# Optimization experiments

Measured on AMD Instinct MI355X. Metric: run time of the kernel, lower is better.

## Reference

```python
import jax, jax.numpy as jnp
import numpy as np
from jax import lax

NEG = -1.0e9


def setup_inputs() -> dict:
    key = jax.random.key(0)
    ks = jax.random.split(key, 12)
    B, S, d, H = 4, 1024, 1024, 16
    sc = 1.0 / np.sqrt(d)
    inp = {
        "query": jax.random.normal(ks[0], (B, S, d), jnp.float32),
        "key": jax.random.normal(ks[1], (B, S, d), jnp.float32),
        "value": jax.random.normal(ks[2], (B, S, d), jnp.float32),
        # causal mask: True = masked (future positions)
        "mask": jnp.triu(jnp.ones((S, S), bool), k=1)[None, None],
        "Wq": jax.random.normal(ks[3], (d, d), jnp.float32) * sc,
        "bq": jnp.zeros((d,), jnp.float32),
        "Wk": jax.random.normal(ks[4], (d, d), jnp.float32) * sc,
        "bk": jnp.zeros((d,), jnp.float32),
        "Wv": jax.random.normal(ks[5], (d, d), jnp.float32) * sc,
        "bv": jnp.zeros((d,), jnp.float32),
        "Wo": jax.random.normal(ks[6], (d, d), jnp.float32) * sc,
        "bo": jnp.zeros((d,), jnp.float32),
        "gammas": jax.random.uniform(ks[7], (H, 1, 1), jnp.float32, -0.05, 0.05),
    }
    return inp


def reference(query, key, value, mask, Wq, bq, Wk, bk, Wv, bv, Wo, bo, gammas):
    B, S, d = query.shape
    H = gammas.shape[0]
    dk = d // H

    def proj(x, W, b):
        # [B,S,d] -> [B,H,S,dk]
        return (x @ W.T + b).reshape(B, S, H, dk).transpose(0, 2, 1, 3)

    q = proj(query, Wq, bq)
    k = proj(key, Wk, bk)
    v = proj(value, Wv, bv)

    scores = jnp.einsum("bhqd,bhkd->bhqk", q, k) / np.float32(np.sqrt(dk))

    # --- distance-decay effect (no-grad block in torch) ---
    p = jax.nn.softmax(jnp.where(mask, NEG, scores), axis=-1)
    distcum = jnp.cumsum(p, axis=-1)
    disttot = jnp.sum(p, axis=-1, keepdims=True)
    idx = jnp.arange(S, dtype=scores.dtype)
    pos = jnp.abs(idx[:, None] - idx[None, :])[None, None]  # [1,1,S,S]
    dist = jnp.sqrt(jnp.clip((disttot - distcum) * pos, 0.0))
    dist = lax.stop_gradient(dist)

    gamma = -jnp.abs(gammas)[None]  # [1,H,1,1]
    total_effect = jnp.clip(jnp.exp(dist * gamma), 1e-5, 1e5)

    gated = jnp.where(mask, NEG, scores * total_effect)
    attn = jax.nn.softmax(gated, axis=-1)
    attn = jnp.where(mask, 0.0, attn)

    out = jnp.einsum("bhqk,bhkd->bhqd", attn, v)
    out = out.transpose(0, 2, 1, 3).reshape(B, S, d)
    out = out @ Wo.T + bo
    return out, attn
```

## Files before the change

### kernel.cpp

```cpp
#include <hip/hip_runtime.h>
#include <hip/hip_bf16.h>

typedef __attribute__((ext_vector_type(8))) short short8;
typedef __attribute__((ext_vector_type(4))) float f32x4;
typedef __attribute__((ext_vector_type(4))) unsigned short us4;

#define MFMA(a, b, c) __builtin_amdgcn_mfma_f32_16x16x32_bf16((a), (b), (c), 0, 0, 0)

static __device__ inline unsigned short f2b(float f) {
    __hip_bfloat16 h = __float2bfloat16(f);
    return *reinterpret_cast<unsigned short*>(&h);
}
static __device__ inline float b2f(unsigned short u) {
    unsigned int x = ((unsigned int)u) << 16;
    return __builtin_bit_cast(float, x);
}

static __device__ __forceinline__ void gload_lds16(const unsigned short* g, unsigned short* s) {
    __builtin_amdgcn_global_load_lds(
        (const __attribute__((address_space(1))) unsigned int*)(g),
        (__attribute__((address_space(3))) unsigned int*)(s),
        16, 0, 0);
}
#define WAITV(N) asm volatile("s_waitcnt vmcnt(" #N ")" ::: "memory")
#define WAITL    asm volatile("s_waitcnt lgkmcnt(0)" ::: "memory")
#define SBAR     __builtin_amdgcn_s_barrier()
#define SCHED0   __builtin_amdgcn_sched_barrier(0)

__global__ __launch_bounds__(256) void convk(
    const float* __restrict__ i0, const float* __restrict__ i1,
    const float* __restrict__ i2, const float* __restrict__ i3,
    unsigned short* o0, unsigned short* o1, unsigned short* o2, unsigned short* o3, int n)
{
    const float* in; unsigned short* out;
    switch (blockIdx.y) {
        case 0: in = i0; out = o0; break;
        case 1: in = i1; out = o1; break;
        case 2: in = i2; out = o2; break;
        default: in = i3; out = o3; break;
    }
    int i = (blockIdx.x * 256 + threadIdx.x) * 4;
    if (i >= n) return;
    float4 v = *(const float4*)(in + i);
    us4 o;
    o[0] = f2b(v.x); o[1] = f2b(v.y); o[2] = f2b(v.z); o[3] = f2b(v.w);
    *(us4*)(out + i) = o;
}

__global__ __launch_bounds__(256) void gemm_qkv(
    const float* __restrict__ Aq, const float* __restrict__ Ak, const float* __restrict__ Av,
    const unsigned short* __restrict__ wq, const unsigned short* __restrict__ wk,
    const unsigned short* __restrict__ wv,
    const float* __restrict__ bq, const float* __restrict__ bk, const float* __restrict__ bv,
    unsigned short* __restrict__ qh, unsigned short* __restrict__ kh,
    unsigned short* __restrict__ vt,
    int M, int N, int K)
{
    __shared__ unsigned short sA[3][2 * 64 * 32];
    __shared__ unsigned short sB[3][2 * 128 * 32];

    const int d  = blockIdx.x;
    const int c  = d & 7;
    const int t  = d >> 3;
    const int nn = t & 7;
    const int gq = t >> 3;
    const int g  = gq * 8 + c;
    const int z  = g >> 6;
    const int mm = g & 63;

    const float* A           = z == 0 ? Aq : z == 1 ? Ak : Av;
    const unsigned short* Bm = z == 0 ? wq : z == 1 ? wk : wv;
    const float* bias        = z == 0 ? bq : z == 1 ? bk : bv;
    unsigned short* Cb       = z == 0 ? qh : z == 1 ? kh : vt;
    const int emode          = z == 2 ? 2 : 1;

    const int tid = threadIdx.x;
    const int wave = tid >> 6, lane = tid & 63;
    const int wm = (wave >> 1) * 32, wn = (wave & 1) * 64;
    const int bm = mm * 64, bn = nn * 128;
    const int fr = lane & 15, fg = lane >> 4;

    const int ar = tid >> 2, ac = (tid & 3) * 16;
    const float* Ag = A + (size_t)(bm + ar) * K + ac;
    const int aks = ac >> 5, acol = ac & 31;
    const int brow = lane >> 2, bchk = (lane & 3) * 8;
    const unsigned short* Bg = Bm + (size_t)(bn + wave * 32 + brow) * K + bchk;

    f32x4 acc[2][4] = {};
    const int nt = K >> 6;

    float4 rA[4];
    #define LOAD_A(t)  { const float* p = Ag + ((t) << 6); \
        rA[0] = *(const float4*)(p); rA[1] = *(const float4*)(p + 4); \
        rA[2] = *(const float4*)(p + 8); rA[3] = *(const float4*)(p + 12); }
    #define GLOAD_B(buf, t) { const unsigned short* p = Bg + ((t) << 6); \
        gload_lds16(p,               &sB[buf][(0 * 128 + wave * 32 + 0 ) * 32]); \
        gload_lds16(p + 16 * K,      &sB[buf][(0 * 128 + wave * 32 + 16) * 32]); \
        gload_lds16(p + 32,          &sB[buf][(1 * 128 + wave * 32 + 0 ) * 32]); \
        gload_lds16(p + 16 * K + 32, &sB[buf][(1 * 128 + wave * 32 + 16) * 32]); }
    #define WRITE_A(buf) { \
        unsigned short* dsts = &sA[buf][(aks * 64 + ar) * 32 + acol]; \
        us4 w0, w1; \
        w0[0] = f2b(rA[0].x); w0[1] = f2b(rA[0].y); w0[2] = f2b(rA[0].z); w0[3] = f2b(rA[0].w); \
        w1[0] = f2b(rA[1].x); w1[1] = f2b(rA[1].y); w1[2] = f2b(rA[1].z); w1[3] = f2b(rA[1].w); \
        *(us4*)(dsts) = w0; *(us4*)(dsts + 4) = w1; \
        w0[0] = f2b(rA[2].x); w0[1] = f2b(rA[2].y); w0[2] = f2b(rA[2].z); w0[3] = f2b(rA[2].w); \
        w1[0] = f2b(rA[3].x); w1[1] = f2b(rA[3].y); w1[2] = f2b(rA[3].z); w1[3] = f2b(rA[3].w); \
        *(us4*)(dsts + 8) = w0; *(us4*)(dsts + 12) = w1; }

    LOAD_A(0);
    SCHED0;
    GLOAD_B(0, 0);
    WAITV(4);
    WRITE_A(0);
    LOAD_A(1);
    SCHED0;
    GLOAD_B(1, 1);

    for (int t = 0; t < nt; ++t) {
        const int cur = t % 3;
        if (t + 1 < nt) { WAITV(4); } else { WAITV(0); }
        if (t + 1 < nt) { WRITE_A((t + 1) % 3); }
        if (t + 2 < nt) {
            LOAD_A(t + 2);
            SCHED0;
            GLOAD_B((t + 2) % 3, t + 2);
        }
        WAITL;
        SBAR; SCHED0;

        short8 af[2][2], bf[4][2];
        #pragma unroll
        for (int ks = 0; ks < 2; ++ks) {
            #pragma unroll
            for (int mr = 0; mr < 2; ++mr)
                af[mr][ks] = *(const short8*)&sA[cur][(ks * 64 + wm + mr * 16 + fr) * 32 + fg * 8];
            #pragma unroll
            for (int nr = 0; nr < 4; ++nr)
                bf[nr][ks] = *(const short8*)&sB[cur][(ks * 128 + wn + nr * 16 + fr) * 32 + fg * 8];
        }
        #pragma unroll
        for (int ks = 0; ks < 2; ++ks)
            #pragma unroll
            for (int mr = 0; mr < 2; ++mr)
                #pragma unroll
                for (int nr = 0; nr < 4; ++nr)
                    acc[mr][nr] = MFMA(af[mr][ks], bf[nr][ks], acc[mr][nr]);

        SCHED0; SBAR;
    }

    #pragma unroll
    for (int mr = 0; mr < 2; ++mr)
        #pragma unroll
        for (int nr = 0; nr < 4; ++nr)
            #pragma unroll
            for (int j = 0; j < 4; ++j) {
                int m = bm + wm + mr * 16 + fg * 4 + j;
                int n = bn + wn + nr * 16 + fr;
                float v = acc[mr][nr][j] + bias[n];
                int b = m >> 10, s = m & 1023, h = n >> 6, dc = n & 63;
                if (emode == 1)
                    Cb[(((size_t)(b * 16 + h)) * 1024 + s) * 64 + dc] = f2b(v);
                else
                    Cb[(((size_t)(b * 16 + h)) * 64 + dc) * 1024 + s] = f2b(v);
            }
    #undef LOAD_A
    #undef GLOAD_B
    #undef WRITE_A
}

__global__ __launch_bounds__(256) void gemm_wo(
    const unsigned short* __restrict__ A, const unsigned short* __restrict__ Bm,
    const float* __restrict__ bias, float* __restrict__ Cf, int M, int N, int K)
{
    __shared__ unsigned short sA[3][2 * 64 * 32];
    __shared__ unsigned short sB[3][2 * 128 * 32];

    const int d  = blockIdx.x;
    const int c  = d & 7;
    const int t0 = d >> 3;
    const int nn = t0 & 7;
    const int gq = t0 >> 3;
    const int mm = gq * 8 + c;

    const int tid = threadIdx.x;
    const int wave = tid >> 6, lane = tid & 63;
    const int wm = (wave >> 1) * 32, wn = (wave & 1) * 64;
    const int bm = mm * 64, bn = nn * 128;
    const int fr = lane & 15, fg = lane >> 4;

    const int srow = lane >> 2, schk = (lane & 3) * 8;
    const unsigned short* Ag = A + (size_t)(bm + wave * 16 + srow) * K + schk;
    const unsigned short* Bg = Bm + (size_t)(bn + wave * 32 + srow) * K + schk;

    #define STAGE(buf, t) { const unsigned short* ap = Ag + ((t) << 6); \
        gload_lds16(ap,      &sA[buf][(0 * 64 + wave * 16) * 32]); \
        gload_lds16(ap + 32, &sA[buf][(1 * 64 + wave * 16) * 32]); \
        const unsigned short* bp = Bg + ((t) << 6); \
        gload_lds16(bp,               &sB[buf][(0 * 128 + wave * 32 + 0 ) * 32]); \
        gload_lds16(bp + 16 * K,      &sB[buf][(0 * 128 + wave * 32 + 16) * 32]); \
        gload_lds16(bp + 32,          &sB[buf][(1 * 128 + wave * 32 + 0 ) * 32]); \
        gload_lds16(bp + 16 * K + 32, &sB[buf][(1 * 128 + wave * 32 + 16) * 32]); }

    f32x4 acc[2][4] = {};
    const int nt = K >> 6;

    STAGE(0, 0); STAGE(1, 1);
    for (int t = 0; t < nt; ++t) {
        const int cur = t % 3;
        if (t + 2 < nt)      { STAGE((t + 2) % 3, t + 2); WAITV(12); }
        else if (t + 1 < nt) { WAITV(6); }
        else                 { WAITV(0); }
        SBAR; SCHED0;

        short8 af[2][2], bf[4][2];
        #pragma unroll
        for (int ks = 0; ks < 2; ++ks) {
            #pragma unroll
            for (int mr = 0; mr < 2; ++mr)
                af[mr][ks] = *(const short8*)&sA[cur][(ks * 64 + wm + mr * 16 + fr) * 32 + fg * 8];
            #pragma unroll
            for (int nr = 0; nr < 4; ++nr)
                bf[nr][ks] = *(const short8*)&sB[cur][(ks * 128 + wn + nr * 16 + fr) * 32 + fg * 8];
        }
        #pragma unroll
        for (int ks = 0; ks < 2; ++ks)
            #pragma unroll
            for (int mr = 0; mr < 2; ++mr)
                #pragma unroll
                for (int nr = 0; nr < 4; ++nr)
                    acc[mr][nr] = MFMA(af[mr][ks], bf[nr][ks], acc[mr][nr]);

        SCHED0; SBAR;
    }
    #undef STAGE

    #pragma unroll
    for (int mr = 0; mr < 2; ++mr)
        #pragma unroll
        for (int nr = 0; nr < 4; ++nr)
            #pragma unroll
            for (int j = 0; j < 4; ++j) {
                int m = bm + wm + mr * 16 + fg * 4 + j;
                int n = bn + wn + nr * 16 + fr;
                Cf[(size_t)m * N + n] = acc[mr][nr][j] + bias[n];
            }
}

__global__ __launch_bounds__(256) void attn_fused(
    const unsigned short* __restrict__ Qh,
    const unsigned short* __restrict__ Kh,
    const unsigned short* __restrict__ Vt,
    const float* __restrict__ gammas,
    float* __restrict__ attn_out,
    unsigned short* __restrict__ ctx)
{
    extern __shared__ char smem[];
    const int RS = 1032;
    unsigned short* s_s = (unsigned short*)smem;
    unsigned short* s_q = (unsigned short*)(smem + 16 * RS * 2);
    float* s_inv = (float*)(smem + 16 * RS * 2 + 16 * 72 * 2);
    const int S = 1024;

    int gid = blockIdx.y * gridDim.x + blockIdx.x;
    int jj = gid >> 3;
    const int bh = (gid & 7) * 8 + (jj >> 6);
    const int qb = jj & 63;
    const int q0 = qb * 16;
    const int tid = threadIdx.x;
    const int wave = tid >> 6, lane = tid & 63, fr = lane & 15, fg = lane >> 4;

    {
        int rr = tid >> 4, c4 = (tid & 15) * 4;
        *(uint2*)&s_q[rr * 72 + c4] = *(const uint2*)&Qh[((size_t)bh * S + q0 + rr) * 64 + c4];
    }
    __syncthreads();
    const int kmax = q0 + 15;

    {
        short8 qf0 = *(const short8*)&s_q[fr * 72 + fg * 8];
        short8 qf1 = *(const short8*)&s_q[fr * 72 + 32 + fg * 8];
        const unsigned short* kbase = &Kh[(size_t)bh * S * 64];
        for (int nf = 0; nf < 16; ++nf) {
            int cb = (nf * 4 + wave) * 16;
            if (cb > kmax) break;
            const unsigned short* kb = kbase + (size_t)cb * 64;
            short8 kf0 = *(const short8*)&kb[fr * 64 + fg * 8];
            short8 kf1 = *(const short8*)&kb[fr * 64 + 32 + fg * 8];
            f32x4 a = {0.f, 0.f, 0.f, 0.f};
            a = MFMA(qf0, kf0, a);
            a = MFMA(qf1, kf1, a);
            #pragma unroll
            for (int j = 0; j < 4; ++j)
                s_s[(size_t)(fg * 4 + j) * RS + cb + fr] = f2b(a[j] * 0.125f);
        }
    }
    __syncthreads();

    {
        const int r = tid >> 4, sub = tid & 15;
        const int qr = q0 + r;
        unsigned short* srow = &s_s[(size_t)r * RS];
        const float ag = fabsf(gammas[bh & 15]);
        const int m = ((qb + 4) >> 2) | 1;
        const int L = 4 * m;
        const int base = sub * L;

        float seg = 0.f;
        for (int c = 0; c < m; ++c) {
            us4 s4 = *(const us4*)&srow[base + c * 4];
            #pragma unroll
            for (int j = 0; j < 4; ++j) {
                int kk = base + c * 4 + j;
                seg += (kk <= qr) ? __expf(b2f(s4[j])) : 0.f;
            }
        }
        float x = seg, t;
        t = __shfl_up(x, 1, 16); if (sub >= 1) x += t;
        t = __shfl_up(x, 2, 16); if (sub >= 2) x += t;
        t = __shfl_up(x, 4, 16); if (sub >= 4) x += t;
        t = __shfl_up(x, 8, 16); if (sub >= 8) x += t;
        const float T = __shfl(x, 15, 16);
        const float invT = 1.f / T;
        float run = x - seg;

        float ls2 = 0.f;
        for (int c = 0; c < m; ++c) {
            us4 s4 = *(const us4*)&srow[base + c * 4];
            us4 o;
            #pragma unroll
            for (int j = 0; j < 4; ++j) {
                int kk = base + c * 4 + j;
                bool act = kk <= qr;
                float s = b2f(s4[j]);
                float e = act ? __expf(s) : 0.f;
                run += e;
                float rem = fmaxf(T - run, 0.f) * invT;
                float dist = sqrtf(rem * (float)(qr - kk));
                float te = __expf(-ag * dist);
                float e2 = act ? __expf(s * te) : 0.f;
                o[j] = f2b(e2);
                ls2 += e2;
            }
            *(us4*)&srow[base + c * 4] = o;
        }
        us4 z = {0, 0, 0, 0};
        for (int c = 4 * L + sub; c < 256; c += 16)
            *(us4*)&srow[c * 4] = z;
        #pragma unroll
        for (int mm = 1; mm < 16; mm <<= 1) ls2 += __shfl_xor(ls2, mm, 16);
        if (sub == 0) s_inv[r] = 1.f / ls2;
    }
    __syncthreads();

    for (int r2 = 0; r2 < 16; ++r2) {
        us4 e4 = *(const us4*)&s_s[(size_t)r2 * RS + tid * 4];
        float iv = s_inv[r2];
        f32x4 w = {b2f(e4[0]) * iv, b2f(e4[1]) * iv, b2f(e4[2]) * iv, b2f(e4[3]) * iv};
        __builtin_nontemporal_store(w,
            (f32x4*)(attn_out + ((size_t)bh * S + q0 + r2) * S + tid * 4));
    }

    {
        const unsigned short* vb = &Vt[(size_t)bh * 64 * S];
        f32x4 acc = {0.f, 0.f, 0.f, 0.f};
        const int ktiles = (kmax + 32) >> 5;
        const unsigned short* prow = &s_s[(size_t)fr * RS];
        for (int kt = 0; kt < ktiles; ++kt) {
            short8 pa = *(const short8*)&prow[kt * 32 + fg * 8];
            short8 vf = *(const short8*)&vb[(size_t)(wave * 16 + fr) * S + kt * 32 + fg * 8];
            acc = MFMA(pa, vf, acc);
        }
        int b = bh >> 4, h = bh & 15;
        #pragma unroll
        for (int j = 0; j < 4; ++j) {
            float iv = s_inv[fg * 4 + j];
            ctx[((size_t)b * S + q0 + fg * 4 + j) * 1024 + h * 64 + wave * 16 + fr] = f2b(acc[j] * iv);
        }
    }
}

extern "C" void kernel_launch(void* const* d_in, const int* in_sizes, int n_in,
                              void* d_out, int out_size, void* d_ws, size_t ws_size,
                              hipStream_t stream) {
    const float* query  = (const float*)d_in[0];
    const float* key    = (const float*)d_in[1];
    const float* value  = (const float*)d_in[2];
    const float* Wq = (const float*)d_in[4];
    const float* bq = (const float*)d_in[5];
    const float* Wk = (const float*)d_in[6];
    const float* bk = (const float*)d_in[7];
    const float* Wv = (const float*)d_in[8];
    const float* bv = (const float*)d_in[9];
    const float* Wo = (const float*)d_in[10];
    const float* bo = (const float*)d_in[11];
    const float* gammas = (const float*)d_in[12];

    const int S = 1024, dmodel = 1024;
    const int M = 4 * S;
    const size_t MD = (size_t)M * dmodel;
    const size_t DD = (size_t)dmodel * dmodel;

    char* ws = (char*)d_ws;
    unsigned short* wqb = (unsigned short*)ws;            ws += DD * 2;
    unsigned short* wkb = (unsigned short*)ws;            ws += DD * 2;
    unsigned short* wvb = (unsigned short*)ws;            ws += DD * 2;
    unsigned short* wob = (unsigned short*)ws;            ws += DD * 2;
    unsigned short* qh  = (unsigned short*)ws;            ws += MD * 2;
    unsigned short* kh  = (unsigned short*)ws;            ws += MD * 2;
    unsigned short* vt  = (unsigned short*)ws;            ws += MD * 2;
    unsigned short* ctx = (unsigned short*)ws;            ws += MD * 2;

    float* outp = (float*)d_out;
    float* attn_out = outp + MD;

    convk<<<dim3(1024, 4), 256, 0, stream>>>(Wq, Wk, Wv, Wo, wqb, wkb, wvb, wob, (int)DD);

    gemm_qkv<<<dim3(1536), 256, 0, stream>>>(
        query, key, value, wqb, wkb, wvb, bq, bk, bv, qh, kh, vt, M, dmodel, dmodel);

    size_t lds = 16 * 1032 * 2 + 16 * 72 * 2 + 16 * 4;
    attn_fused<<<dim3(64, 64), 256, lds, stream>>>(qh, kh, vt, gammas, attn_out, ctx);

    gemm_wo<<<dim3(512), 256, 0, stream>>>(ctx, wob, bo, outp, M, dmodel, dmodel);
}
```

Before: 184.6 us.

## Halve GEMM K-tile to 32 and use exp2 with log2e-prescaled scores

Both projection GEMMs now stage 32-wide K tiles instead of 64, which halves shared-memory buffers and per-stage loads but doubles the number of loop iterations and barriers. The attention softmax/decay path folds log2(e) into the score scale and gamma, so it can call the hardware exp2 directly instead of __expf. This removes multiplies from the exp-heavy inner loop and lowers LDS usage, which may raise GEMM occupancy. The cost is more per-iteration sync overhead in the GEMMs. Storing scores in bf16 after scaling by log2(e) also changes rounding slightly.

```diff
diff --git a/kernel.cpp b/kernel.cpp
--- a/kernel.cpp
+++ b/kernel.cpp
@@ -6,6 +6,7 @@
 typedef __attribute__((ext_vector_type(4))) unsigned short us4;
 
 #define MFMA(a, b, c) __builtin_amdgcn_mfma_f32_16x16x32_bf16((a), (b), (c), 0, 0, 0)
+#define EXP2(x) __builtin_amdgcn_exp2f(x)
 
 static __device__ inline unsigned short f2b(float f) {
     __hip_bfloat16 h = __float2bfloat16(f);
@@ -56,15 +57,14 @@
     unsigned short* __restrict__ vt,
     int M, int N, int K)
 {
-    __shared__ unsigned short sA[3][2 * 64 * 32];
-    __shared__ unsigned short sB[3][2 * 128 * 32];
+    __shared__ unsigned short sA[3][64 * 32];
+    __shared__ unsigned short sB[3][128 * 32];
 
     const int d  = blockIdx.x;
     const int c  = d & 7;
-    const int t  = d >> 3;
-    const int nn = t & 7;
-    const int gq = t >> 3;
-    const int g  = gq * 8 + c;
+    const int t0 = d >> 3;
+    const int nn = t0 & 7;
+    const int g  = (t0 >> 3) * 8 + c;
     const int z  = g >> 6;
     const int mm = g & 63;
 
@@ -80,38 +80,30 @@
     const int bm = mm * 64, bn = nn * 128;
     const int fr = lane & 15, fg = lane >> 4;
 
-    const int ar = tid >> 2, ac = (tid & 3) * 16;
+    const int ar = tid >> 2, ac = (tid & 3) * 8;
     const float* Ag = A + (size_t)(bm + ar) * K + ac;
-    const int aks = ac >> 5, acol = ac & 31;
-    const int brow = lane >> 2, bchk = (lane & 3) * 8;
-    const unsigned short* Bg = Bm + (size_t)(bn + wave * 32 + brow) * K + bchk;
+    const unsigned short* Bg = Bm + (size_t)(bn + wave * 32 + (lane >> 2)) * K + (lane & 3) * 8;
 
     f32x4 acc[2][4] = {};
-    const int nt = K >> 6;
-
-    float4 rA[4];
-    #define LOAD_A(t)  { const float* p = Ag + ((t) << 6); \
-        rA[0] = *(const float4*)(p); rA[1] = *(const float4*)(p + 4); \
-        rA[2] = *(const float4*)(p + 8); rA[3] = *(const float4*)(p + 12); }
-    #define GLOAD_B(buf, t) { const unsigned short* p = Bg + ((t) << 6); \
-        gload_lds16(p,               &sB[buf][(0 * 128 + wave * 32 + 0 ) * 32]); \
-        gload_lds16(p + 16 * K,      &sB[buf][(0 * 128 + wave * 32 + 16) * 32]); \
-        gload_lds16(p + 32,          &sB[buf][(1 * 128 + wave * 32 + 0 ) * 32]); \
-        gload_lds16(p + 16 * K + 32, &sB[buf][(1 * 128 + wave * 32 + 16) * 32]); }
+    const int nt = K >> 5;
+
+    float4 rA[2];
+    #define LOAD_A(t)  { const float* p = Ag + ((t) << 5); \
+        rA[0] = *(const float4*)(p); rA[1] = *(const float4*)(p + 4); }
+    #define GLOAD_B(buf, t) { const unsigned short* p = Bg + ((t) << 5); \
+        gload_lds16(p,          &sB[buf][(wave * 32 + 0 ) * 32]); \
+        gload_lds16(p + 16 * K, &sB[buf][(wave * 32 + 16) * 32]); }
     #define WRITE_A(buf) { \
-        unsigned short* dsts = &sA[buf][(aks * 64 + ar) * 32 + acol]; \
+        unsigned short* dsts = &sA[buf][ar * 32 + ac]; \
         us4 w0, w1; \
         w0[0] = f2b(rA[0].x); w0[1] = f2b(rA[0].y); w0[2] = f2b(rA[0].z); w0[3] = f2b(rA[0].w); \
         w1[0] = f2b(rA[1].x); w1[1] = f2b(rA[1].y); w1[2] = f2b(rA[1].z); w1[3] = f2b(rA[1].w); \
-        *(us4*)(dsts) = w0; *(us4*)(dsts + 4) = w1; \
-        w0[0] = f2b(rA[2].x); w0[1] = f2b(rA[2].y); w0[2] = f2b(rA[2].z); w0[3] = f2b(rA[2].w); \
-        w1[0] = f2b(rA[3].x); w1[1] = f2b(rA[3].y); w1[2] = f2b(rA[3].z); w1[3] = f2b(rA[3].w); \
-        *(us4*)(dsts + 8) = w0; *(us4*)(dsts + 12) = w1; }
+        *(us4*)(dsts) = w0; *(us4*)(dsts + 4) = w1; }
 
     LOAD_A(0);
     SCHED0;
     GLOAD_B(0, 0);
-    WAITV(4);
+    WAITV(2);
     WRITE_A(0);
     LOAD_A(1);
     SCHED0;
@@ -119,7 +111,7 @@
 
     for (int t = 0; t < nt; ++t) {
         const int cur = t % 3;
-        if (t + 1 < nt) { WAITV(4); } else { WAITV(0); }
+        if (t + 1 < nt) { WAITV(2); } else { WAITV(0); }
         if (t + 1 < nt) { WRITE_A((t + 1) % 3); }
         if (t + 2 < nt) {
             LOAD_A(t + 2);
@@ -129,23 +121,18 @@
         WAITL;
         SBAR; SCHED0;
 
-        short8 af[2][2], bf[4][2];
-        #pragma unroll
-        for (int ks = 0; ks < 2; ++ks) {
-            #pragma unroll
-            for (int mr = 0; mr < 2; ++mr)
-                af[mr][ks] = *(const short8*)&sA[cur][(ks * 64 + wm + mr * 16 + fr) * 32 + fg * 8];
+        short8 af[2], bf[4];
+        #pragma unroll
+        for (int mr = 0; mr < 2; ++mr)
+            af[mr] = *(const short8*)&sA[cur][(wm + mr * 16 + fr) * 32 + fg * 8];
+        #pragma unroll
+        for (int nr = 0; nr < 4; ++nr)
+            bf[nr] = *(const short8*)&sB[cur][(wn + nr * 16 + fr) * 32 + fg * 8];
+        #pragma unroll
+        for (int mr = 0; mr < 2; ++mr)
             #pragma unroll
             for (int nr = 0; nr < 4; ++nr)
-                bf[nr][ks] = *(const short8*)&sB[cur][(ks * 128 + wn + nr * 16 + fr) * 32 + fg * 8];
-        }
-        #pragma unroll
-        for (int ks = 0; ks < 2; ++ks)
-            #pragma unroll
-            for (int mr = 0; mr < 2; ++mr)
-                #pragma unroll
-                for (int nr = 0; nr < 4; ++nr)
-                    acc[mr][nr] = MFMA(af[mr][ks], bf[nr][ks], acc[mr][nr]);
+                acc[mr][nr] = MFMA(af[mr], bf[nr], acc[mr][nr]);
 
         SCHED0; SBAR;
     }
@@ -174,15 +161,14 @@
     const unsigned short* __restrict__ A, const unsigned short* __restrict__ Bm,
     const float* __restrict__ bias, float* __restrict__ Cf, int M, int N, int K)
 {
-    __shared__ unsigned short sA[3][2 * 64 * 32];
-    __shared__ unsigned short sB[3][2 * 128 * 32];
+    __shared__ unsigned short sA[3][64 * 32];
+    __shared__ unsigned short sB[3][128 * 32];
 
     const int d  = blockIdx.x;
     const int c  = d & 7;
     const int t0 = d >> 3;
     const int nn = t0 & 7;
-    const int gq = t0 >> 3;
-    const int mm = gq * 8 + c;
+    const int mm = (t0 >> 3) * 8 + c;
 
     const int tid = threadIdx.x;
     const int wave = tid >> 6, lane = tid & 63;
@@ -190,47 +176,38 @@
     const int bm = mm * 64, bn = nn * 128;
     const int fr = lane & 15, fg = lane >> 4;
 
-    const int srow = lane >> 2, schk = (lane & 3) * 8;
-    const unsigned short* Ag = A + (size_t)(bm + wave * 16 + srow) * K + schk;
-    const unsigned short* Bg = Bm + (size_t)(bn + wave * 32 + srow) * K + schk;
-
-    #define STAGE(buf, t) { const unsigned short* ap = Ag + ((t) << 6); \
-        gload_lds16(ap,      &sA[buf][(0 * 64 + wave * 16) * 32]); \
-        gload_lds16(ap + 32, &sA[buf][(1 * 64 + wave * 16) * 32]); \
-        const unsigned short* bp = Bg + ((t) << 6); \
-        gload_lds16(bp,               &sB[buf][(0 * 128 + wave * 32 + 0 ) * 32]); \
-        gload_lds16(bp + 16 * K,      &sB[buf][(0 * 128 + wave * 32 + 16) * 32]); \
-        gload_lds16(bp + 32,          &sB[buf][(1 * 128 + wave * 32 + 0 ) * 32]); \
-        gload_lds16(bp + 16 * K + 32, &sB[buf][(1 * 128 + wave * 32 + 16) * 32]); }
+    const unsigned short* Ag = A + (size_t)(bm + wave * 16 + (lane >> 2)) * K + (lane & 3) * 8;
+    const unsigned short* Bg = Bm + (size_t)(bn + wave * 32 + (lane >> 2)) * K + (lane & 3) * 8;
+
+    #define STAGE(buf, t) { \
+        gload_lds16(Ag + ((t) << 5),          &sA[buf][(wave * 16) * 32]); \
+        const unsigned short* bp = Bg + ((t) << 5); \
+        gload_lds16(bp,          &sB[buf][(wave * 32 + 0 ) * 32]); \
+        gload_lds16(bp + 16 * K, &sB[buf][(wave * 32 + 16) * 32]); }
 
     f32x4 acc[2][4] = {};
-    const int nt = K >> 6;
+    const int nt = K >> 5;
 
     STAGE(0, 0); STAGE(1, 1);
     for (int t = 0; t < nt; ++t) {
         const int cur = t % 3;
-        if (t + 2 < nt)      { STAGE((t + 2) % 3, t + 2); WAITV(12); }
-        else if (t + 1 < nt) { WAITV(6); }
+        if (t + 2 < nt)      { STAGE((t + 2) % 3, t + 2); WAITV(6); }
+        else if (t + 1 < nt) { WAITV(3); }
         else                 { WAITV(0); }
         SBAR; SCHED0;
 
-        short8 af[2][2], bf[4][2];
-        #pragma unroll
-        for (int ks = 0; ks < 2; ++ks) {
-            #pragma unroll
-            for (int mr = 0; mr < 2; ++mr)
-                af[mr][ks] = *(const short8*)&sA[cur][(ks * 64 + wm + mr * 16 + fr) * 32 + fg * 8];
+        short8 af[2], bf[4];
+        #pragma unroll
+        for (int mr = 0; mr < 2; ++mr)
+            af[mr] = *(const short8*)&sA[cur][(wm + mr * 16 + fr) * 32 + fg * 8];
+        #pragma unroll
+        for (int nr = 0; nr < 4; ++nr)
+            bf[nr] = *(const short8*)&sB[cur][(wn + nr * 16 + fr) * 32 + fg * 8];
+        #pragma unroll
+        for (int mr = 0; mr < 2; ++mr)
             #pragma unroll
             for (int nr = 0; nr < 4; ++nr)
-                bf[nr][ks] = *(const short8*)&sB[cur][(ks * 128 + wn + nr * 16 + fr) * 32 + fg * 8];
-        }
-        #pragma unroll
-        for (int ks = 0; ks < 2; ++ks)
-            #pragma unroll
-            for (int mr = 0; mr < 2; ++mr)
-                #pragma unroll
-                for (int nr = 0; nr < 4; ++nr)
-                    acc[mr][nr] = MFMA(af[mr][ks], bf[nr][ks], acc[mr][nr]);
+                acc[mr][nr] = MFMA(af[mr], bf[nr], acc[mr][nr]);
 
         SCHED0; SBAR;
     }
@@ -293,7 +270,7 @@
             a = MFMA(qf1, kf1, a);
             #pragma unroll
             for (int j = 0; j < 4; ++j)
-                s_s[(size_t)(fg * 4 + j) * RS + cb + fr] = f2b(a[j] * 0.125f);
+                s_s[(size_t)(fg * 4 + j) * RS + cb + fr] = f2b(a[j] * 0.18033688f);
         }
     }
     __syncthreads();
@@ -302,7 +279,7 @@
         const int r = tid >> 4, sub = tid & 15;
         const int qr = q0 + r;
         unsigned short* srow = &s_s[(size_t)r * RS];
-        const float ag = fabsf(gammas[bh & 15]);
+        const float ag2 = fabsf(gammas[bh & 15]) * 1.44269504f;
         const int m = ((qb + 4) >> 2) | 1;
         const int L = 4 * m;
         const int base = sub * L;
@@ -313,7 +290,7 @@
             #pragma unroll
             for (int j = 0; j < 4; ++j) {
                 int kk = base + c * 4 + j;
-                seg += (kk <= qr) ? __expf(b2f(s4[j])) : 0.f;
+                seg += (kk <= qr) ? EXP2(b2f(s4[j])) : 0.f;
             }
         }
         float x = seg, t;
@@ -333,13 +310,13 @@
             for (int j = 0; j < 4; ++j) {
                 int kk = base + c * 4 + j;
                 bool act = kk <= qr;
-                float s = b2f(s4[j]);
-                float e = act ? __expf(s) : 0.f;
+                float u = b2f(s4[j]);
+                float e = act ? EXP2(u) : 0.f;
                 run += e;
                 float rem = fmaxf(T - run, 0.f) * invT;
                 float dist = sqrtf(rem * (float)(qr - kk));
-                float te = __expf(-ag * dist);
-                float e2 = act ? __expf(s * te) : 0.f;
+                float te = EXP2(-ag2 * dist);
+                float e2 = act ? EXP2(u * te) : 0.f;
                 o[j] = f2b(e2);
                 ls2 += e2;
             }
```

Result: no change. 185.2 us (+0.3%).
